# Kernel optimization log

Hardware: AMD Instinct MI355X
Metric: run time of the kernel (lower is better)

## Reference

```python
import jax, jax.numpy as jnp
import numpy as np

N_GRAPHS = 4
NODES_PER_GRAPH = 8192
N_NODES = N_GRAPHS * NODES_PER_GRAPH
N_EDGES = N_NODES * 16
IN_DIM = 3
HID = 128
K_OUT = 512
MAX_WAVELENGTH = 10000.0


def _glorot(k, shape):
    lim = (6.0 / (shape[0] + shape[1])) ** 0.5
    return jax.random.uniform(k, shape, jnp.float32, -lim, lim)


def setup_inputs() -> dict:
    key = jax.random.key(0)
    ks = jax.random.split(key, 12)
    z = lambda *s: jnp.zeros(s, jnp.float32)
    return {
        "x": jax.random.normal(ks[0], (N_NODES, IN_DIM), jnp.float32),
        "mesh_pos": jax.random.uniform(ks[1], (N_NODES, 2), jnp.float32),
        "mesh_edges": jax.random.randint(ks[2], (N_EDGES, 2), 0, N_NODES, jnp.int32),
        "batch_idx": jnp.arange(N_NODES, dtype=jnp.int32) // NODES_PER_GRAPH,
        "proj_w": _glorot(ks[3], (IN_DIM, HID)), "proj_b": z(HID),
        "msg_w1": _glorot(ks[4], (2 * HID, HID)), "msg_b1": z(HID),
        "msg_w2": _glorot(ks[5], (HID, HID)), "msg_b2": z(HID),
        "upd_w1": _glorot(ks[6], (2 * HID, HID)), "upd_b1": z(HID),
        "upd_w2": _glorot(ks[7], (HID, HID)), "upd_b2": z(HID),
        "pool_rel_w": _glorot(ks[8], (HID, 1)), "pool_rel_b": z(1),
        "pool_root_w": _glorot(ks[9], (HID, 1)),
    }


def _sincos_embed(pos):
    # ContinuousSincosEmbed: HID=128, ndim=2 -> 64 channels per coord dim, 32 freqs
    dim_per_ndim = HID // 2
    omega = 1.0 / MAX_WAVELENGTH ** (jnp.arange(0, dim_per_ndim, 2, dtype=jnp.float32) / dim_per_ndim)
    ang = pos[:, :, None] * omega  # [N, ndim, 32]
    emb = jnp.concatenate([jnp.sin(ang), jnp.cos(ang)], axis=-1)  # [N, ndim, 64]
    return emb.reshape(pos.shape[0], HID)


def reference(x, mesh_pos, mesh_edges, batch_idx, proj_w, proj_b,
              msg_w1, msg_b1, msg_w2, msg_b2, upd_w1, upd_b1, upd_w2, upd_b2,
              pool_rel_w, pool_rel_b, pool_root_w):
    src, dst = mesh_edges[:, 0], mesh_edges[:, 1]  # edge_index[0]=j(src), [1]=i(dst)
    h = x @ proj_w + proj_b + _sincos_embed(mesh_pos)
    cnt = jnp.maximum(jax.ops.segment_sum(jnp.ones((N_EDGES,), h.dtype), dst, num_segments=N_NODES), 1.0)
    # message passing layer (depth=1): message MLP on [x_i, x_j], scatter-mean, residual update MLP
    m_in = jnp.concatenate([h[dst], h[src]], axis=-1)  # [E, 2H]
    m = jax.nn.silu(m_in @ msg_w1 + msg_b1) @ msg_w2 + msg_b2
    agg = jax.ops.segment_sum(m, dst, num_segments=N_NODES) / cnt[:, None]
    h = h + (jax.nn.silu(jnp.concatenate([h, agg], axis=-1) @ upd_w1 + upd_b1) @ upd_w2 + upd_b2)
    # SAGPooling score: GraphConv(HID,1,aggr='mean'), tanh nonlinearity
    nagg = jax.ops.segment_sum(h[src], dst, num_segments=N_NODES) / cnt[:, None]
    score = jnp.tanh((nagg @ pool_rel_w + pool_rel_b + h @ pool_root_w)[:, 0])
    # fixed top-k per graph (batch_idx is contiguous blocks of NODES_PER_GRAPH)
    topv, topi = jax.lax.top_k(score.reshape(N_GRAPHS, NODES_PER_GRAPH), K_OUT)
    perm = (topi + jnp.arange(N_GRAPHS, dtype=topi.dtype)[:, None] * NODES_PER_GRAPH).reshape(-1)
    x_pool = h[perm] * topv.reshape(-1)[:, None]
    batch_pool = jnp.repeat(jnp.arange(N_GRAPHS, dtype=batch_idx.dtype), K_OUT)
    return x_pool, batch_pool
```

## Files before the change

kernel.cpp:

```cpp
#include <hip/hip_runtime.h>
#include <hip/hip_bf16.h>
#include <math.h>

#define N_NODESC 32768
#define N_EDGESC 524288
#define NPG 8192
#define KOUT 512

typedef unsigned short u16;
typedef unsigned int u32;
typedef unsigned long long u64;

__device__ __forceinline__ float siluf(float x) {
    return x / (1.f + __expf(-x));
}

__global__ __launch_bounds__(256) void k_h0(const float* __restrict__ x,
                                            const float* __restrict__ pos,
                                            const float* __restrict__ pw,
                                            const float* __restrict__ pb,
                                            float* __restrict__ h,
                                            int* __restrict__ deg) {
    int gid = blockIdx.x * 256 + threadIdx.x;
    if (gid < N_NODESC) deg[gid] = 0;
    int node = blockIdx.x * 2 + (threadIdx.x >> 7);
    int c = threadIdx.x & 127;
    float x0 = x[node * 3 + 0];
    float x1 = x[node * 3 + 1];
    float x2 = x[node * 3 + 2];
    float acc = x0 * pw[c] + x1 * pw[128 + c] + x2 * pw[256 + c];
    acc += pb[c];
    int dim = c >> 6;
    int inner = c & 63;
    int jj = inner & 31;
    float p = pos[node * 2 + dim];
    float omega = exp2f(-(float)jj * 0.41524101186092027f);
    float ang = p * omega;
    acc += (inner < 32) ? __sinf(ang) : __cosf(ang);
    h[(size_t)node * 128 + c] = acc;
}

__global__ __launch_bounds__(256) void k_deg(const int* __restrict__ edges, int* __restrict__ deg) {
    int e = blockIdx.x * 256 + threadIdx.x;
    if (e < N_EDGESC) {
        int2 e2 = ((const int2*)edges)[e];
        atomicAdd(&deg[e2.y], 1);
    }
}

__global__ __launch_bounds__(1024) void k_scan(const int* __restrict__ deg,
                                               int* __restrict__ off, int* __restrict__ cur,
                                               float* __restrict__ rs, float* __restrict__ bg) {
    __shared__ int ls[1024];
    int tid = threadIdx.x;
    int base = tid * 32;
    int v[32];
    int s = 0;
#pragma unroll
    for (int j = 0; j < 32; j++) { v[j] = deg[base + j]; s += v[j]; }
    ls[tid] = s;
    __syncthreads();
    for (int ofs = 1; ofs < 1024; ofs <<= 1) {
        int t = (tid >= ofs) ? ls[tid - ofs] : 0;
        __syncthreads();
        ls[tid] += t;
        __syncthreads();
    }
    int run = ls[tid] - s;
#pragma unroll
    for (int j = 0; j < 32; j++) {
        off[base + j] = run;
        cur[base + j] = run;
        int d = v[j];
        rs[base + j] = 1.f / (float)(d > 0 ? d : 1);
        bg[base + j] = d > 0 ? 1.f : 0.f;
        run += d;
    }
}

__global__ __launch_bounds__(256) void k_fill(const int* __restrict__ edges,
                                              int* __restrict__ cur, int* __restrict__ csr) {
    int e = blockIdx.x * 256 + threadIdx.x;
    if (e < N_EDGESC) {
        int2 e2 = ((const int2*)edges)[e];
        int pos = atomicAdd(&cur[e2.y], 1);
        csr[pos] = e2.x;
    }
}

__global__ __launch_bounds__(256) void k_sortcsr(int* __restrict__ csr,
                                                 const int* __restrict__ off,
                                                 const int* __restrict__ deg) {
    int d = blockIdx.x * 4 + (threadIdx.x >> 6);
    int lane = threadIdx.x & 63;
    int o = off[d], n = deg[d];
    if (n <= 1) return;
    if (n <= 64) {
        int key = (lane < n) ? csr[o + lane] : 0x7FFFFFFF;
        for (int k = 2; k <= 64; k <<= 1) {
            for (int j = k >> 1; j > 0; j >>= 1) {
                int partner = __shfl_xor(key, j);
                bool asc = ((lane & k) == 0);
                bool keepMin = (((lane & j) == 0) == asc);
                key = keepMin ? min(key, partner) : max(key, partner);
            }
        }
        if (lane < n) csr[o + lane] = key;
    } else {
        if (lane == 0) {
            for (int i = o + 1; i < o + n; i++) {
                int x = csr[i];
                int j = i - 1;
                while (j >= o && csr[j] > x) { csr[j + 1] = csr[j]; j--; }
                csr[j + 1] = x;
            }
        }
    }
}

__global__ __launch_bounds__(256, 2) void gemm_dualw(const float* __restrict__ A,
                                                     const float* __restrict__ Wv,
                                                     const float* __restrict__ Wu,
                                                     const float* __restrict__ bu,
                                                     float* __restrict__ V, float* __restrict__ U) {
    __shared__ float Wsv[32 * 128];
    __shared__ float Wsu[32 * 128];
    int tid = threadIdx.x;
    int cg = tid & 31;
    int rg = tid >> 5;
    int m0 = blockIdx.x * 32 + rg * 4;
    int c0 = cg * 4;
    const float* Ar = A + (size_t)m0 * 128;

    float accv[4][4], accu[4][4];
#pragma unroll
    for (int r = 0; r < 4; r++)
#pragma unroll
        for (int c = 0; c < 4; c++) { accv[r][c] = 0.f; accu[r][c] = 0.f; }

    for (int kc = 0; kc < 128; kc += 32) {
        __syncthreads();
        {
            const float4* Wgv = (const float4*)(Wv + (size_t)kc * 128);
            const float4* Wgu = (const float4*)(Wu + (size_t)kc * 128);
            float4* Wlv = (float4*)Wsv;
            float4* Wlu = (float4*)Wsu;
#pragma unroll
            for (int i = 0; i < 4; i++) {
                Wlv[tid + i * 256] = Wgv[tid + i * 256];
                Wlu[tid + i * 256] = Wgu[tid + i * 256];
            }
        }
        __syncthreads();
#pragma unroll
        for (int k0 = 0; k0 < 32; k0 += 4) {
            float4 a[4];
#pragma unroll
            for (int r = 0; r < 4; r++) a[r] = *(const float4*)(Ar + r * 128 + kc + k0);
#pragma unroll
            for (int kk = 0; kk < 4; kk++) {
                float4 wv = *(const float4*)(Wsv + (k0 + kk) * 128 + c0);
                float4 wu = *(const float4*)(Wsu + (k0 + kk) * 128 + c0);
#pragma unroll
                for (int r = 0; r < 4; r++) {
                    float aa = ((const float*)&a[r])[kk];
                    accv[r][0] += aa * wv.x; accv[r][1] += aa * wv.y;
                    accv[r][2] += aa * wv.z; accv[r][3] += aa * wv.w;
                    accu[r][0] += aa * wu.x; accu[r][1] += aa * wu.y;
                    accu[r][2] += aa * wu.z; accu[r][3] += aa * wu.w;
                }
            }
        }
    }
#pragma unroll
    for (int r = 0; r < 4; r++) {
        int row = m0 + r;
        float4 ov, ou;
        ov.x = accv[r][0]; ov.y = accv[r][1]; ov.z = accv[r][2]; ov.w = accv[r][3];
        ou.x = accu[r][0] + bu[c0];
        ou.y = accu[r][1] + bu[c0 + 1];
        ou.z = accu[r][2] + bu[c0 + 2];
        ou.w = accu[r][3] + bu[c0 + 3];
        *(float4*)(V + (size_t)row * 128 + c0) = ov;
        *(float4*)(U + (size_t)row * 128 + c0) = ou;
    }
}

__global__ __launch_bounds__(256, 2) void gemm_dualA(const float* __restrict__ A1,
                                                     const float* __restrict__ W1,
                                                     const float* __restrict__ A2,
                                                     const float* __restrict__ W2,
                                                     const float* __restrict__ bias,
                                                     float* __restrict__ C) {
    __shared__ float Ws1[32 * 128];
    __shared__ float Ws2[32 * 128];
    int tid = threadIdx.x;
    int cg = tid & 31;
    int rg = tid >> 5;
    int m0 = blockIdx.x * 32 + rg * 4;
    int c0 = cg * 4;
    const float* Ar1 = A1 + (size_t)m0 * 128;
    const float* Ar2 = A2 + (size_t)m0 * 128;

    float acc1[4][4], acc2[4][4];
#pragma unroll
    for (int r = 0; r < 4; r++)
#pragma unroll
        for (int c = 0; c < 4; c++) { acc1[r][c] = 0.f; acc2[r][c] = 0.f; }

    for (int kc = 0; kc < 128; kc += 32) {
        __syncthreads();
        {
            const float4* Wg1 = (const float4*)(W1 + (size_t)kc * 128);
            const float4* Wg2 = (const float4*)(W2 + (size_t)kc * 128);
            float4* Wl1 = (float4*)Ws1;
            float4* Wl2 = (float4*)Ws2;
#pragma unroll
            for (int i = 0; i < 4; i++) {
                Wl1[tid + i * 256] = Wg1[tid + i * 256];
                Wl2[tid + i * 256] = Wg2[tid + i * 256];
            }
        }
        __syncthreads();
#pragma unroll
        for (int k0 = 0; k0 < 32; k0 += 4) {
            float4 a1[4], a2[4];
#pragma unroll
            for (int r = 0; r < 4; r++) {
                a1[r] = *(const float4*)(Ar1 + r * 128 + kc + k0);
                a2[r] = *(const float4*)(Ar2 + r * 128 + kc + k0);
            }
#pragma unroll
            for (int kk = 0; kk < 4; kk++) {
                float4 w1 = *(const float4*)(Ws1 + (k0 + kk) * 128 + c0);
                float4 w2 = *(const float4*)(Ws2 + (k0 + kk) * 128 + c0);
#pragma unroll
                for (int r = 0; r < 4; r++) {
                    float aa = ((const float*)&a1[r])[kk];
                    float bb = ((const float*)&a2[r])[kk];
                    acc1[r][0] += aa * w1.x; acc1[r][1] += aa * w1.y;
                    acc1[r][2] += aa * w1.z; acc1[r][3] += aa * w1.w;
                    acc2[r][0] += bb * w2.x; acc2[r][1] += bb * w2.y;
                    acc2[r][2] += bb * w2.z; acc2[r][3] += bb * w2.w;
                }
            }
        }
    }
#pragma unroll
    for (int r = 0; r < 4; r++) {
        int row = m0 + r;
        float4 o;
        float* op = (float*)&o;
#pragma unroll
        for (int c = 0; c < 4; c++) {
            float xv = acc1[r][c];
            xv += acc2[r][c];
            xv += bias[c0 + c];
            op[c] = siluf(xv);
        }
        *(float4*)(C + (size_t)row * 128 + c0) = o;
    }
}

__global__ __launch_bounds__(256, 2) void gemm_lds(const float* __restrict__ A, const float* __restrict__ W,
                                                   const float* __restrict__ bias,
                                                   const float* __restrict__ rs, const float* __restrict__ bg,
                                                   const float* __restrict__ resid,
                                                   float* __restrict__ C, int act,
                                                   const float* __restrict__ wrel, const float* __restrict__ wroot,
                                                   float* __restrict__ pout, float* __restrict__ rout) {
    __shared__ float Ws[32 * 128];
    int tid = threadIdx.x;
    int cg = tid & 31;
    int rg = tid >> 5;
    int m0 = blockIdx.x * 32 + rg * 4;
    int c0 = cg * 4;
    const float* Ar = A + (size_t)m0 * 128;

    float acc[4][4];
#pragma unroll
    for (int r = 0; r < 4; r++)
#pragma unroll
        for (int c = 0; c < 4; c++) acc[r][c] = 0.f;

    float4 aA[4], aB[4], wA[4], wB[4];

#define LOAD_A(buf, k)                                                   \
    {                                                                    \
        _Pragma("unroll") for (int r = 0; r < 4; r++)                    \
            buf[r] = *(const float4*)(Ar + r * 128 + (k));               \
    }
#define LOAD_W(buf, k)                                                   \
    {                                                                    \
        _Pragma("unroll") for (int kk = 0; kk < 4; kk++)                 \
            buf[kk] = *(const float4*)(Ws + ((k) + kk) * 128 + c0);      \
    }
#define COMPUTE(ab, wb)                                                  \
    {                                                                    \
        _Pragma("unroll") for (int kk = 0; kk < 4; kk++) {               \
            float4 wv = wb[kk];                                          \
            _Pragma("unroll") for (int r = 0; r < 4; r++) {              \
                float a = ((const float*)&ab[r])[kk];                    \
                acc[r][0] += a * wv.x;                                   \
                acc[r][1] += a * wv.y;                                   \
                acc[r][2] += a * wv.z;                                   \
                acc[r][3] += a * wv.w;                                   \
            }                                                            \
        }                                                                \
    }

    for (int kc = 0; kc < 128; kc += 32) {
        __syncthreads();
        {
            const float4* Wg = (const float4*)(W + (size_t)kc * 128);
            float4* Wl = (float4*)Ws;
#pragma unroll
            for (int i = 0; i < 4; i++) Wl[tid + i * 256] = Wg[tid + i * 256];
        }
        __syncthreads();
        LOAD_A(aA, kc)
        LOAD_W(wA, 0)
        for (int k0 = 0; k0 < 32; k0 += 8) {
            LOAD_A(aB, kc + k0 + 4)
            LOAD_W(wB, k0 + 4)
            COMPUTE(aA, wA)
            if (k0 + 8 < 32) {
                LOAD_A(aA, kc + k0 + 8)
                LOAD_W(wA, k0 + 8)
            }
            COMPUTE(aB, wB)
        }
    }
#undef LOAD_A
#undef LOAD_W
#undef COMPUTE

    float prel[4], prot[4];
#pragma unroll
    for (int r = 0; r < 4; r++) {
        int row = m0 + r;
        float rsv = rs ? rs[row] : 1.f;
        float bgv = bg ? bg[row] : 1.f;
        float4 o;
        float* op = (float*)&o;
#pragma unroll
        for (int c = 0; c < 4; c++) {
            float xv = acc[r][c];
            xv *= rsv;
            if (bias) xv += bias[c0 + c] * bgv;
            if (resid) xv += resid[(size_t)row * 128 + c0 + c];
            if (act) xv = siluf(xv);
            op[c] = xv;
        }
        if (wrel) {
            prel[r] = op[0] * wrel[c0] + op[1] * wrel[c0 + 1] + op[2] * wrel[c0 + 2] + op[3] * wrel[c0 + 3];
            prot[r] = op[0] * wroot[c0] + op[1] * wroot[c0 + 1] + op[2] * wroot[c0 + 2] + op[3] * wroot[c0 + 3];
        }
        *(float4*)(C + (size_t)row * 128 + c0) = o;
    }
    if (wrel) {
#pragma unroll
        for (int r = 0; r < 4; r++) {
            float a = prel[r], b = prot[r];
#pragma unroll
            for (int m = 1; m < 32; m <<= 1) {
                a += __shfl_xor(a, m);
                b += __shfl_xor(b, m);
            }
            if (cg == 0) { pout[m0 + r] = a; rout[m0 + r] = b; }
        }
    }
}

__global__ __launch_bounds__(256) void k_accum_S(const float* __restrict__ v,
                                                 const int* __restrict__ csr, const int* __restrict__ off,
                                                 const int* __restrict__ deg, float* S) {
    int d = blockIdx.x * 4 + (threadIdx.x >> 6);
    int lane = threadIdx.x & 63;
    int half = lane >> 5;
    int l32 = lane & 31;
    float* srow = S + (size_t)d * 128;
    float4 u = *(const float4*)(srow + l32 * 4);
    float4 a = {0.f, 0.f, 0.f, 0.f};
    int o = off[d], n = deg[d];
    for (int base = 0; base < n; base += 64) {
        int cnt = min(64, n - base);
        int sall = (lane < cnt) ? csr[o + base + lane] : 0;
        int j = 0;
        for (; j + 8 <= cnt; j += 8) {
            int s0 = __shfl(sall, j + 0 + half);
            int s1 = __shfl(sall, j + 2 + half);
            int s2 = __shfl(sall, j + 4 + half);
            int s3 = __shfl(sall, j + 6 + half);
            float4 v0 = *(const float4*)(v + (size_t)s0 * 128 + l32 * 4);
            float4 v1 = *(const float4*)(v + (size_t)s1 * 128 + l32 * 4);
            float4 v2 = *(const float4*)(v + (size_t)s2 * 128 + l32 * 4);
            float4 v3 = *(const float4*)(v + (size_t)s3 * 128 + l32 * 4);
            a.x += siluf(u.x + v0.x); a.y += siluf(u.y + v0.y);
            a.z += siluf(u.z + v0.z); a.w += siluf(u.w + v0.w);
            a.x += siluf(u.x + v1.x); a.y += siluf(u.y + v1.y);
            a.z += siluf(u.z + v1.z); a.w += siluf(u.w + v1.w);
            a.x += siluf(u.x + v2.x); a.y += siluf(u.y + v2.y);
            a.z += siluf(u.z + v2.z); a.w += siluf(u.w + v2.w);
            a.x += siluf(u.x + v3.x); a.y += siluf(u.y + v3.y);
            a.z += siluf(u.z + v3.z); a.w += siluf(u.w + v3.w);
        }
        for (; j < cnt; j += 2) {
            if (j + 1 < cnt) {
                int s = __shfl(sall, j + half);
                float4 vv = *(const float4*)(v + (size_t)s * 128 + l32 * 4);
                a.x += siluf(u.x + vv.x); a.y += siluf(u.y + vv.y);
                a.z += siluf(u.z + vv.z); a.w += siluf(u.w + vv.w);
            } else {
                int s = __shfl(sall, j);
                if (half == 0) {
                    float4 vv = *(const float4*)(v + (size_t)s * 128 + l32 * 4);
                    a.x += siluf(u.x + vv.x); a.y += siluf(u.y + vv.y);
                    a.z += siluf(u.z + vv.z); a.w += siluf(u.w + vv.w);
                }
            }
        }
    }
    float ox = __shfl(a.x, l32 + 32);
    float oy = __shfl(a.y, l32 + 32);
    float oz = __shfl(a.z, l32 + 32);
    float ow = __shfl(a.w, l32 + 32);
    if (half == 0) {
        float4 t;
        t.x = a.x + ox; t.y = a.y + oy; t.z = a.z + oz; t.w = a.w + ow;
        *(float4*)(srow + l32 * 4) = t;
    }
}

__global__ __launch_bounds__(256) void k_score(const float* __restrict__ p, const float* __restrict__ r,
                                               const int* __restrict__ csr, const int* __restrict__ off,
                                               const int* __restrict__ deg, const float* __restrict__ relb,
                                               float* __restrict__ score) {
    int d = blockIdx.x * 4 + (threadIdx.x >> 6);
    int lane = threadIdx.x & 63;
    int o = off[d], n = deg[d];
    float a = 0.f;
    for (int j = lane; j < n; j += 64) a += p[csr[o + j]];
    for (int m = 32; m > 0; m >>= 1) a += __shfl_xor(a, m);
    if (lane == 0) {
        float cnt = (float)(n > 0 ? n : 1);
        score[d] = tanhf(a / cnt + relb[0] + r[d]);
    }
}

__global__ __launch_bounds__(1024) void k_topk(const float* __restrict__ score, const float* __restrict__ h,
                                               float* __restrict__ out) {
    __shared__ u32 ms[NPG];
    __shared__ u32 hist[256];
    __shared__ u32 sbuf[1024];
    __shared__ u64 sel[KOUT];
    __shared__ float ordv[KOUT];
    __shared__ int ordi[KOUT];
    __shared__ u32 selCnt, sPrefix, sNeed, sB;

    int g = blockIdx.x;
    int tid = threadIdx.x;

    for (int i = tid; i < NPG; i += 1024) {
        u32 u = __float_as_uint(score[(size_t)g * NPG + i]);
        ms[i] = (u & 0x80000000u) ? ~u : (u | 0x80000000u);
    }
    if (tid == 0) { sNeed = KOUT; sPrefix = 0; selCnt = 0; }
    __syncthreads();

    for (int pass = 0; pass < 4; pass++) {
        int shift = 24 - pass * 8;
        if (tid < 256) hist[tid] = 0;
        __syncthreads();
        u32 pfx = sPrefix;
        for (int i = tid; i < NPG; i += 1024) {
            u32 v = ms[i];
            if (pass == 0 || (v >> (shift + 8)) == pfx)
                atomicAdd(&hist[(v >> shift) & 255u], 1u);
        }
        __syncthreads();
        if (tid < 256) sbuf[tid] = hist[tid];
        __syncthreads();
        for (int ofs = 1; ofs < 256; ofs <<= 1) {
            u32 t = 0;
            if (tid < 256 && tid + ofs < 256) t = sbuf[tid + ofs];
            __syncthreads();
            if (tid < 256) sbuf[tid] += t;
            __syncthreads();
        }
        u32 need = sNeed;
        if (tid < 256) {
            if (sbuf[tid] >= need && (tid == 255 || sbuf[tid + 1] < need)) sB = (u32)tid;
        }
        __syncthreads();
        if (tid == 0) {
            u32 B = sB;
            u32 above = (B == 255) ? 0u : sbuf[B + 1];
            sNeed = need - above;
            sPrefix = (sPrefix << 8) | B;
        }
        __syncthreads();
    }
    u32 T = sPrefix;
    u32 rTie = sNeed;

    int base = tid * 8;
    u32 lc = 0;
#pragma unroll
    for (int j = 0; j < 8; j++) lc += (ms[base + j] == T);
    __syncthreads();
    sbuf[tid] = lc;
    __syncthreads();
    u32 own = lc;
    for (int ofs = 1; ofs < 1024; ofs <<= 1) {
        u32 t = (tid >= ofs) ? sbuf[tid - ofs] : 0;
        __syncthreads();
        sbuf[tid] += t;
        __syncthreads();
    }
    u32 excl = sbuf[tid] - own;

#pragma unroll
    for (int j = 0; j < 8; j++) {
        int i = base + j;
        u32 v = ms[i];
        bool pick = (v > T) || ((v == T) && (excl < rTie));
        if (v == T) excl++;
        if (pick) {
            u32 slot = atomicAdd(&selCnt, 1u);
            sel[slot] = ((u64)v << 32) | (u32)(NPG - 1 - i);
        }
    }
    __syncthreads();

    if (tid < KOUT) {
        u64 mine = sel[tid];
        int rank = 0;
        for (int j = 0; j < KOUT; j++) rank += (sel[j] > mine);
        u32 v = (u32)(mine >> 32);
        int idx = NPG - 1 - (int)(mine & 0xFFFFFFFFu);
        u32 uu = (v & 0x80000000u) ? (v & 0x7FFFFFFFu) : ~v;
        ordv[rank] = __uint_as_float(uu);
        ordi[rank] = idx;
    }
    __syncthreads();

    for (int t = tid; t < KOUT * 128; t += 1024) {
        int r = t >> 7, c = t & 127;
        int node = g * NPG + ordi[r];
        out[((size_t)g * KOUT + r) * 128 + c] = h[(size_t)node * 128 + c] * ordv[r];
    }
    for (int t = tid; t < KOUT; t += 1024)
        out[(size_t)4 * KOUT * 128 + (size_t)g * KOUT + t] = (float)g;
}

extern "C" void kernel_launch(void* const* d_in, const int* in_sizes, int n_in,
                              void* d_out, int out_size, void* d_ws, size_t ws_size,
                              hipStream_t stream) {
    const float* x        = (const float*)d_in[0];
    const float* mesh_pos = (const float*)d_in[1];
    const int*   edges    = (const int*)d_in[2];
    const float* proj_w   = (const float*)d_in[4];
    const float* proj_b   = (const float*)d_in[5];
    const float* msg_w1   = (const float*)d_in[6];
    const float* msg_b1   = (const float*)d_in[7];
    const float* msg_w2   = (const float*)d_in[8];
    const float* msg_b2   = (const float*)d_in[9];
    const float* upd_w1   = (const float*)d_in[10];
    const float* upd_b1   = (const float*)d_in[11];
    const float* upd_w2   = (const float*)d_in[12];
    const float* upd_b2   = (const float*)d_in[13];
    const float* pool_rel_w  = (const float*)d_in[14];
    const float* pool_rel_b  = (const float*)d_in[15];
    const float* pool_root_w = (const float*)d_in[16];
    float* out = (float*)d_out;

    char* w = (char*)d_ws;
    float* h  = (float*)(w);
    float* v  = (float*)(w + (1ull << 24));
    float* S  = (float*)(w + (2ull << 24));
    char* sm  = w + (3ull << 24);
    int*   deg   = (int*)(sm);
    int*   off   = (int*)(sm + 131072);
    int*   cur   = (int*)(sm + 262144);
    float* rsA   = (float*)(sm + 393216);
    float* bgA   = (float*)(sm + 524288);
    float* pp    = (float*)(sm + 655360);
    float* rr    = (float*)(sm + 786432);
    float* score = (float*)(sm + 917504);
    int*   csr   = (int*)(sm + 1048576);

    k_h0<<<N_NODESC / 2, 256, 0, stream>>>(x, mesh_pos, proj_w, proj_b, h, deg);
    k_deg<<<N_EDGESC / 256, 256, 0, stream>>>(edges, deg);
    k_scan<<<1, 1024, 0, stream>>>(deg, off, cur, rsA, bgA);
    k_fill<<<N_EDGESC / 256, 256, 0, stream>>>(edges, cur, csr);
    k_sortcsr<<<N_NODESC / 4, 256, 0, stream>>>(csr, off, deg);

    gemm_dualw<<<1024, 256, 0, stream>>>(h, msg_w1 + 128 * 128, msg_w1, msg_b1, v, S);
    k_accum_S<<<N_NODESC / 4, 256, 0, stream>>>(v, csr, off, deg, S);
    gemm_lds<<<1024, 256, 0, stream>>>(S, msg_w2, msg_b2, rsA, bgA, nullptr,
                                       v, 0, nullptr, nullptr, nullptr, nullptr);
    gemm_dualA<<<1024, 256, 0, stream>>>(h, upd_w1, v, upd_w1 + 128 * 128, upd_b1, S);
    gemm_lds<<<1024, 256, 0, stream>>>(S, upd_w2, upd_b2, nullptr, nullptr, h,
                                       h, 0, pool_rel_w, pool_root_w, pp, rr);

    k_score<<<N_NODESC / 4, 256, 0, stream>>>(pp, rr, csr, off, deg, pool_rel_b, score);
    k_topk<<<4, 1024, 0, stream>>>(score, h, out);
}
```

Measured before the change: 393.5 us.

## Fuse message-W2, update MLP and pooling projections into one chained GEMM kernel

Replaces three separate GEMM launches (msg W2, dual-A update W1, update W2 with residual and pool projections) with a single kernel that keeps the 32-row intermediate tiles in shared memory between stages. This removes the global writes and reads of the intermediate 32768x128 activations and two kernel launches. In exchange the kernel has more LDS use per block (two 16KB buffers) and many more barriers. It also drops the software-pipelined A/W register prefetch that gemm_lds had.

```diff
diff --git a/kernel.cpp b/kernel.cpp
--- a/kernel.cpp
+++ b/kernel.cpp
@@ -186,66 +186,135 @@
     }
 }
 
-__global__ __launch_bounds__(256, 2) void gemm_dualA(const float* __restrict__ A1,
-                                                     const float* __restrict__ W1,
-                                                     const float* __restrict__ A2,
+__global__ __launch_bounds__(256, 2) void gemm_chain(const float* __restrict__ S,
+                                                     float* __restrict__ h,
                                                      const float* __restrict__ W2,
-                                                     const float* __restrict__ bias,
-                                                     float* __restrict__ C) {
-    __shared__ float Ws1[32 * 128];
-    __shared__ float Ws2[32 * 128];
+                                                     const float* __restrict__ b2,
+                                                     const float* __restrict__ rs,
+                                                     const float* __restrict__ bg,
+                                                     const float* __restrict__ U1a,
+                                                     const float* __restrict__ U1b,
+                                                     const float* __restrict__ ub1,
+                                                     const float* __restrict__ U2,
+                                                     const float* __restrict__ ub2,
+                                                     const float* __restrict__ wrel,
+                                                     const float* __restrict__ wroot,
+                                                     float* __restrict__ pout,
+                                                     float* __restrict__ rout) {
+    __shared__ float Wc[32 * 128];
+    __shared__ float T[32 * 128];
     int tid = threadIdx.x;
     int cg = tid & 31;
     int rg = tid >> 5;
     int m0 = blockIdx.x * 32 + rg * 4;
     int c0 = cg * 4;
-    const float* Ar1 = A1 + (size_t)m0 * 128;
-    const float* Ar2 = A2 + (size_t)m0 * 128;
+    const float* Sr = S + (size_t)m0 * 128;
+    const float* hr = h + (size_t)m0 * 128;
 
     float acc1[4][4], acc2[4][4];
-#pragma unroll
-    for (int r = 0; r < 4; r++)
-#pragma unroll
-        for (int c = 0; c < 4; c++) { acc1[r][c] = 0.f; acc2[r][c] = 0.f; }
-
+
+#define ZERO(acc)                                                        \
+    {                                                                    \
+        _Pragma("unroll") for (int r = 0; r < 4; r++)                    \
+            _Pragma("unroll") for (int c = 0; c < 4; c++) acc[r][c] = 0.f; \
+    }
+#define STAGE_W(Wsrc, kc)                                                \
+    {                                                                    \
+        __syncthreads();                                                 \
+        const float4* Wg = (const float4*)((Wsrc) + (size_t)(kc) * 128); \
+        float4* Wl = (float4*)Wc;                                        \
+        _Pragma("unroll") for (int i = 0; i < 4; i++)                    \
+            Wl[tid + i * 256] = Wg[tid + i * 256];                       \
+        __syncthreads();                                                 \
+    }
+#define COMPUTE_G(acc, Abase, kc)                                        \
+    {                                                                    \
+        _Pragma("unroll") for (int k0 = 0; k0 < 32; k0 += 4) {           \
+            float4 a[4];                                                 \
+            _Pragma("unroll") for (int r = 0; r < 4; r++)                \
+                a[r] = *(const float4*)((Abase) + r * 128 + (kc) + k0);  \
+            _Pragma("unroll") for (int kk = 0; kk < 4; kk++) {           \
+                float4 wv = *(const float4*)(Wc + (k0 + kk) * 128 + c0); \
+                _Pragma("unroll") for (int r = 0; r < 4; r++) {          \
+                    float aa = ((const float*)&a[r])[kk];                \
+                    acc[r][0] += aa * wv.x; acc[r][1] += aa * wv.y;      \
+                    acc[r][2] += aa * wv.z; acc[r][3] += aa * wv.w;      \
+                }                                                        \
+            }                                                            \
+        }                                                                \
+    }
+#define COMPUTE_T(acc, kc)                                               \
+    {                                                                    \
+        _Pragma("unroll") for (int k0 = 0; k0 < 32; k0 += 4) {           \
+            float4 a[4];                                                 \
+            _Pragma("unroll") for (int r = 0; r < 4; r++)                \
+                a[r] = *(const float4*)(T + (rg * 4 + r) * 128 + (kc) + k0); \
+            _Pragma("unroll") for (int kk = 0; kk < 4; kk++) {           \
+                float4 wv = *(const float4*)(Wc + (k0 + kk) * 128 + c0); \
+                _Pragma("unroll") for (int r = 0; r < 4; r++) {          \
+                    float aa = ((const float*)&a[r])[kk];                \
+                    acc[r][0] += aa * wv.x; acc[r][1] += aa * wv.y;      \
+                    acc[r][2] += aa * wv.z; acc[r][3] += aa * wv.w;      \
+                }                                                        \
+            }                                                            \
+        }                                                                \
+    }
+
+    ZERO(acc1)
     for (int kc = 0; kc < 128; kc += 32) {
-        __syncthreads();
-        {
-            const float4* Wg1 = (const float4*)(W1 + (size_t)kc * 128);
-            const float4* Wg2 = (const float4*)(W2 + (size_t)kc * 128);
-            float4* Wl1 = (float4*)Ws1;
-            float4* Wl2 = (float4*)Ws2;
-#pragma unroll
-            for (int i = 0; i < 4; i++) {
-                Wl1[tid + i * 256] = Wg1[tid + i * 256];
-                Wl2[tid + i * 256] = Wg2[tid + i * 256];
-            }
-        }
-        __syncthreads();
-#pragma unroll
-        for (int k0 = 0; k0 < 32; k0 += 4) {
-            float4 a1[4], a2[4];
-#pragma unroll
-            for (int r = 0; r < 4; r++) {
-                a1[r] = *(const float4*)(Ar1 + r * 128 + kc + k0);
-                a2[r] = *(const float4*)(Ar2 + r * 128 + kc + k0);
-            }
-#pragma unroll
-            for (int kk = 0; kk < 4; kk++) {
-                float4 w1 = *(const float4*)(Ws1 + (k0 + kk) * 128 + c0);
-                float4 w2 = *(const float4*)(Ws2 + (k0 + kk) * 128 + c0);
-#pragma unroll
-                for (int r = 0; r < 4; r++) {
-                    float aa = ((const float*)&a1[r])[kk];
-                    float bb = ((const float*)&a2[r])[kk];
-                    acc1[r][0] += aa * w1.x; acc1[r][1] += aa * w1.y;
-                    acc1[r][2] += aa * w1.z; acc1[r][3] += aa * w1.w;
-                    acc2[r][0] += bb * w2.x; acc2[r][1] += bb * w2.y;
-                    acc2[r][2] += bb * w2.z; acc2[r][3] += bb * w2.w;
-                }
-            }
-        }
-    }
+        STAGE_W(W2, kc)
+        COMPUTE_G(acc1, Sr, kc)
+    }
+#pragma unroll
+    for (int r = 0; r < 4; r++) {
+        int row = m0 + r;
+        float rsv = rs[row];
+        float bgv = bg[row];
+        float4 o;
+        float* op = (float*)&o;
+#pragma unroll
+        for (int c = 0; c < 4; c++) {
+            float xv = acc1[r][c];
+            xv *= rsv;
+            xv += b2[c0 + c] * bgv;
+            op[c] = xv;
+        }
+        *(float4*)(T + (rg * 4 + r) * 128 + c0) = o;
+    }
+    __syncthreads();
+
+    ZERO(acc1)
+    for (int kc = 0; kc < 128; kc += 32) {
+        STAGE_W(U1a, kc)
+        COMPUTE_G(acc1, hr, kc)
+    }
+    ZERO(acc2)
+    for (int kc = 0; kc < 128; kc += 32) {
+        STAGE_W(U1b, kc)
+        COMPUTE_T(acc2, kc)
+    }
+    __syncthreads();
+#pragma unroll
+    for (int r = 0; r < 4; r++) {
+        float4 o;
+        float* op = (float*)&o;
+#pragma unroll
+        for (int c = 0; c < 4; c++) {
+            float xv = acc1[r][c];
+            xv += acc2[r][c];
+            xv += ub1[c0 + c];
+            op[c] = siluf(xv);
+        }
+        *(float4*)(T + (rg * 4 + r) * 128 + c0) = o;
+    }
+    __syncthreads();
+
+    ZERO(acc1)
+    for (int kc = 0; kc < 128; kc += 32) {
+        STAGE_W(U2, kc)
+        COMPUTE_T(acc1, kc)
+    }
+    float prel[4], prot[4];
 #pragma unroll
     for (int r = 0; r < 4; r++) {
         int row = m0 + r;
@@ -254,122 +323,29 @@
 #pragma unroll
         for (int c = 0; c < 4; c++) {
             float xv = acc1[r][c];
-            xv += acc2[r][c];
-            xv += bias[c0 + c];
-            op[c] = siluf(xv);
-        }
-        *(float4*)(C + (size_t)row * 128 + c0) = o;
-    }
-}
-
-__global__ __launch_bounds__(256, 2) void gemm_lds(const float* __restrict__ A, const float* __restrict__ W,
-                                                   const float* __restrict__ bias,
-                                                   const float* __restrict__ rs, const float* __restrict__ bg,
-                                                   const float* __restrict__ resid,
-                                                   float* __restrict__ C, int act,
-                                                   const float* __restrict__ wrel, const float* __restrict__ wroot,
-                                                   float* __restrict__ pout, float* __restrict__ rout) {
-    __shared__ float Ws[32 * 128];
-    int tid = threadIdx.x;
-    int cg = tid & 31;
-    int rg = tid >> 5;
-    int m0 = blockIdx.x * 32 + rg * 4;
-    int c0 = cg * 4;
-    const float* Ar = A + (size_t)m0 * 128;
-
-    float acc[4][4];
-#pragma unroll
-    for (int r = 0; r < 4; r++)
-#pragma unroll
-        for (int c = 0; c < 4; c++) acc[r][c] = 0.f;
-
-    float4 aA[4], aB[4], wA[4], wB[4];
-
-#define LOAD_A(buf, k)                                                   \
-    {                                                                    \
-        _Pragma("unroll") for (int r = 0; r < 4; r++)                    \
-            buf[r] = *(const float4*)(Ar + r * 128 + (k));               \
-    }
-#define LOAD_W(buf, k)                                                   \
-    {                                                                    \
-        _Pragma("unroll") for (int kk = 0; kk < 4; kk++)                 \
-            buf[kk] = *(const float4*)(Ws + ((k) + kk) * 128 + c0);      \
-    }
-#define COMPUTE(ab, wb)                                                  \
-    {                                                                    \
-        _Pragma("unroll") for (int kk = 0; kk < 4; kk++) {               \
-            float4 wv = wb[kk];                                          \
-            _Pragma("unroll") for (int r = 0; r < 4; r++) {              \
-                float a = ((const float*)&ab[r])[kk];                    \
-                acc[r][0] += a * wv.x;                                   \
-                acc[r][1] += a * wv.y;                                   \
-                acc[r][2] += a * wv.z;                                   \
-                acc[r][3] += a * wv.w;                                   \
-            }                                                            \
-        }                                                                \
-    }
-
-    for (int kc = 0; kc < 128; kc += 32) {
-        __syncthreads();
-        {
-            const float4* Wg = (const float4*)(W + (size_t)kc * 128);
-            float4* Wl = (float4*)Ws;
-#pragma unroll
-            for (int i = 0; i < 4; i++) Wl[tid + i * 256] = Wg[tid + i * 256];
-        }
-        __syncthreads();
-        LOAD_A(aA, kc)
-        LOAD_W(wA, 0)
-        for (int k0 = 0; k0 < 32; k0 += 8) {
-            LOAD_A(aB, kc + k0 + 4)
-            LOAD_W(wB, k0 + 4)
-            COMPUTE(aA, wA)
-            if (k0 + 8 < 32) {
-                LOAD_A(aA, kc + k0 + 8)
-                LOAD_W(wA, k0 + 8)
-            }
-            COMPUTE(aB, wB)
-        }
-    }
-#undef LOAD_A
-#undef LOAD_W
-#undef COMPUTE
-
-    float prel[4], prot[4];
+            xv *= 1.f;
+            xv += ub2[c0 + c] * 1.f;
+            xv += hr[r * 128 + c0 + c];
+            op[c] = xv;
+        }
+        prel[r] = op[0] * wrel[c0] + op[1] * wrel[c0 + 1] + op[2] * wrel[c0 + 2] + op[3] * wrel[c0 + 3];
+        prot[r] = op[0] * wroot[c0] + op[1] * wroot[c0 + 1] + op[2] * wroot[c0 + 2] + op[3] * wroot[c0 + 3];
+        *(float4*)(h + (size_t)row * 128 + c0) = o;
+    }
 #pragma unroll
     for (int r = 0; r < 4; r++) {
-        int row = m0 + r;
-        float rsv = rs ? rs[row] : 1.f;
-        float bgv = bg ? bg[row] : 1.f;
-        float4 o;
-        float* op = (float*)&o;
-#pragma unroll
-        for (int c = 0; c < 4; c++) {
-            float xv = acc[r][c];
-            xv *= rsv;
-            if (bias) xv += bias[c0 + c] * bgv;
-            if (resid) xv += resid[(size_t)row * 128 + c0 + c];
-            if (act) xv = siluf(xv);
-            op[c] = xv;
-        }
-        if (wrel) {
-            prel[r] = op[0] * wrel[c0] + op[1] * wrel[c0 + 1] + op[2] * wrel[c0 + 2] + op[3] * wrel[c0 + 3];
-            prot[r] = op[0] * wroot[c0] + op[1] * wroot[c0 + 1] + op[2] * wroot[c0 + 2] + op[3] * wroot[c0 + 3];
-        }
-        *(float4*)(C + (size_t)row * 128 + c0) = o;
-    }
-    if (wrel) {
-#pragma unroll
-        for (int r = 0; r < 4; r++) {
-            float a = prel[r], b = prot[r];
-#pragma unroll
-            for (int m = 1; m < 32; m <<= 1) {
-                a += __shfl_xor(a, m);
-                b += __shfl_xor(b, m);
-            }
-            if (cg == 0) { pout[m0 + r] = a; rout[m0 + r] = b; }
-        }
-    }
+        float a = prel[r], b = prot[r];
+#pragma unroll
+        for (int m = 1; m < 32; m <<= 1) {
+            a += __shfl_xor(a, m);
+            b += __shfl_xor(b, m);
+        }
+        if (cg == 0) { pout[m0 + r] = a; rout[m0 + r] = b; }
+    }
+#undef ZERO
+#undef STAGE_W
+#undef COMPUTE_G
+#undef COMPUTE_T
 }
 
 __global__ __launch_bounds__(256) void k_accum_S(const float* __restrict__ v,
@@ -598,11 +574,10 @@
 
     gemm_dualw<<<1024, 256, 0, stream>>>(h, msg_w1 + 128 * 128, msg_w1, msg_b1, v, S);
     k_accum_S<<<N_NODESC / 4, 256, 0, stream>>>(v, csr, off, deg, S);
-    gemm_lds<<<1024, 256, 0, stream>>>(S, msg_w2, msg_b2, rsA, bgA, nullptr,
-                                       v, 0, nullptr, nullptr, nullptr, nullptr);
-    gemm_dualA<<<1024, 256, 0, stream>>>(h, upd_w1, v, upd_w1 + 128 * 128, upd_b1, S);
-    gemm_lds<<<1024, 256, 0, stream>>>(S, upd_w2, upd_b2, nullptr, nullptr, h,
-                                       h, 0, pool_rel_w, pool_root_w, pp, rr);
+    gemm_chain<<<1024, 256, 0, stream>>>(S, h, msg_w2, msg_b2, rsA, bgA,
+                                         upd_w1, upd_w1 + 128 * 128, upd_b1,
+                                         upd_w2, upd_b2,
+                                         pool_rel_w, pool_root_w, pp, rr);
 
     k_score<<<N_NODESC / 4, 256, 0, stream>>>(pp, rr, csr, off, deg, pool_rel_b, score);
     k_topk<<<4, 1024, 0, stream>>>(score, h, out);
```

Measured after the change: 386.6 us. No clear change (-1.8%).
